# Optimization experiments

Measured on AMD Instinct MI355X. Metric: run time of the kernel, lower is better.

Reference implementation:

```python
import jax, jax.numpy as jnp
import numpy as np


def _scan_dir(x, A, B, reverse):
    """First-order linear recurrence h_i = A*h_{i-1} + B*x_i along last axis (W).
    x: [Bsz, C, H, W]; A, B: [C]. reverse=True scans right-to-left but returns
    states in original index order (matching torch scan_backward)."""
    xs = jnp.moveaxis(x, -1, 0)  # [W, Bsz, C, H]
    Ab = A[None, :, None]
    Bb = B[None, :, None]
    def step(h, xi):
        h = Ab * h + Bb * xi
        return h, h
    h0 = jnp.zeros_like(xs[0])
    _, hs = jax.lax.scan(step, h0, xs, reverse=reverse)
    return jnp.moveaxis(hs, 0, -1)  # [Bsz, C, H, W]


def _conv1x1(x, W, b):
    # x: [B,Cin,H,W], W: [Cout,Cin], b: [Cout]
    return jnp.einsum('bchw,dc->bdhw', x, W) + b[None, :, None, None]


def setup_inputs() -> dict:
    key = jax.random.key(0)
    ks = jax.random.split(key, 10)
    B, C, H, W = 8, 64, 128, 128
    D = 128  # hidden_dim
    return {
        'F_in': jax.random.normal(ks[0], (B, C, H, W), dtype=jnp.float32),
        'prior': jax.random.uniform(ks[1], (B, 1, H, W), dtype=jnp.float32),
        'Wi': jax.random.normal(ks[2], (D, C), dtype=jnp.float32) * 0.05,
        'bi': jnp.zeros((D,), dtype=jnp.float32),
        'A_param': jax.random.normal(ks[3], (D,), dtype=jnp.float32),
        'B_param': jax.random.normal(ks[4], (D,), dtype=jnp.float32),
        'alpha': jnp.float32(0.1),
        'gamma': jnp.float32(0.1),
        'Wf': jax.random.normal(ks[5], (D, 4 * D), dtype=jnp.float32) * 0.05,
        'bf': jnp.zeros((D,), dtype=jnp.float32),
        'Wo': jax.random.normal(ks[6], (C, D), dtype=jnp.float32) * 0.05,
        'bo': jnp.zeros((C,), dtype=jnp.float32),
    }


def reference(F_in, prior, Wi, bi, A_param, B_param, alpha, gamma, Wf, bf, Wo, bo):
    # prior has 1 channel, repeated to C channels (prior already matches HxW)
    prior_r = jnp.broadcast_to(prior, F_in.shape)
    F_mod = F_in + alpha * prior_r
    x = _conv1x1(F_mod, Wi, bi)  # [B, D, H, W]
    A = jnp.tanh(A_param)
    Bp = B_param
    h_lr = _scan_dir(x, A, Bp, reverse=False)
    h_rl = _scan_dir(x, A, Bp, reverse=True)
    xt = jnp.swapaxes(x, 2, 3)  # scan over H axis
    h_tb = jnp.swapaxes(_scan_dir(xt, A, Bp, reverse=False), 2, 3)
    h_bt = jnp.swapaxes(_scan_dir(xt, A, Bp, reverse=True), 2, 3)
    h = jnp.concatenate([h_lr, h_rl, h_tb, h_bt], axis=1)  # [B, 4D, H, W]
    h = _conv1x1(h, Wf, bf)   # fusion -> [B, D, H, W]
    out = _conv1x1(h, Wo, bo)  # output_proj -> [B, C, H, W]
    return F_mod + gamma * out
```

## Files before the change

### kernel.cpp

```cpp
#include <hip/hip_runtime.h>
#include <hip/hip_bf16.h>

typedef unsigned int u32;
typedef unsigned short u16;
typedef float f32x2 __attribute__((ext_vector_type(2)));
typedef float f32x4 __attribute__((ext_vector_type(4)));
using bf16x8 = __attribute__((ext_vector_type(8))) short;
using f32x4v = __attribute__((ext_vector_type(4))) float;

#define DEVINL __device__ __forceinline__

constexpr int SCAN_LDS = 32768;
constexpr int XS = 132;
constexpr int LDS_X = 128 * XS * 2;

DEVINL float bf2f(u16 u) { union { u32 i; float f; } v; v.i = ((u32)u) << 16; return v.f; }
DEVINL float bf2f_lo(u32 u) { union { u32 i; float f; } v; v.i = u << 16; return v.f; }
DEVINL float bf2f_hi(u32 u) { union { u32 i; float f; } v; v.i = u & 0xffff0000u; return v.f; }
DEVINL u16 f2bf(float f) {
  __hip_bfloat16 h = __float2bfloat16(f);
  u16 r; __builtin_memcpy(&r, &h, 2); return r;
}
DEVINL u32 pack2(float a, float b) { return (u32)f2bf(a) | ((u32)f2bf(b) << 16); }

__global__ __launch_bounds__(256) void k_pre(
    const float* __restrict__ Wf, const float* __restrict__ Wo,
    const float* __restrict__ bf_, const float* __restrict__ bo,
    const float* __restrict__ A_param, const float* __restrict__ Wi,
    float* __restrict__ A_t, float* __restrict__ beff,
    u16* __restrict__ Mrow, u16* __restrict__ Wi_bf) {
  const int wg = blockIdx.x, t = threadIdx.x;
  if (wg < 128) {
    const int idx = wg * 256 + t;
    const int cout = idx >> 9;
    const int k = idx & 511;
    float s = 0.f;
    for (int d = 0; d < 128; ++d) s = fmaf(Wo[cout * 128 + d], Wf[d * 512 + k], s);
    const int dir = k >> 7, dm = k & 127;
    Mrow[(dir * 64 + cout) * 128 + dm] = f2bf(s);
  } else if (wg == 128) {
    if (t < 128) A_t[t] = tanhf(A_param[t]);
    if (t < 64) {
      float s = bo[t];
      for (int d = 0; d < 128; ++d) s = fmaf(Wo[t * 128 + d], bf_[d], s);
      beff[t] = s;
    }
  } else {
#pragma unroll
    for (int k = 0; k < 32; ++k) {
      const int i = t + k * 256;
      Wi_bf[i] = f2bf(Wi[i]);
    }
  }
}

extern __shared__ char smem[];

template <bool REV>
DEVINL void scan_local(char* buf, int dp, int chunk, f32x2 A2, f32x2 B2) {
  f32x2 h = { 0.f, 0.f };
  const u32 cb = (u32)(dp * 4);
  const int s = chunk * 32;
  u32 nx[8];
#pragma unroll
  for (int j = 0; j < 8; ++j) {
    const int i = REV ? (127 - (s + j)) : (s + j);
    nx[j] = *(const u32*)(buf + i * 128 + (cb ^ ((u32)((i & 7) << 4))));
  }
  for (int ib = 0; ib < 32; ib += 8) {
    u32 cur[8];
#pragma unroll
    for (int j = 0; j < 8; ++j) cur[j] = nx[j];
    if (ib + 8 < 32) {
#pragma unroll
      for (int j = 0; j < 8; ++j) {
        const int i2 = s + ib + 8 + j;
        const int i = REV ? (127 - i2) : i2;
        nx[j] = *(const u32*)(buf + i * 128 + (cb ^ ((u32)((i & 7) << 4))));
      }
    }
#pragma unroll
    for (int j = 0; j < 8; ++j) {
      const int i2 = s + ib + j;
      const int i = REV ? (127 - i2) : i2;
      const f32x2 xv = { bf2f_lo(cur[j]), bf2f_hi(cur[j]) };
      h = A2 * h + B2 * xv;
      *(u32*)(buf + i * 128 + (cb ^ ((u32)((i & 7) << 4)))) = pack2(h.x, h.y);
    }
  }
}

template <bool REV>
DEVINL void scan_fix(char* buf, int dp, int chunk, f32x2 A2) {
  if (chunk == 0) return;
  f32x2 q = A2;
#pragma unroll
  for (int k = 0; k < 5; ++k) q *= q;
  const u32 cb = (u32)(dp * 4);
  f32x2 C = { 0.f, 0.f };
  for (int k = 0; k < chunk; ++k) {
    const int i2 = k * 32 + 31;
    const int i = REV ? (127 - i2) : i2;
    const u32 v = *(const u32*)(buf + i * 128 + (cb ^ ((u32)((i & 7) << 4))));
    const f32x2 xv = { bf2f_lo(v), bf2f_hi(v) };
    C = C * q + xv;
  }
  f32x2 p = A2;
  const int s = chunk * 32;
  u32 nx[8];
#pragma unroll
  for (int j = 0; j < 8; ++j) {
    const int i = REV ? (127 - (s + j)) : (s + j);
    nx[j] = *(const u32*)(buf + i * 128 + (cb ^ ((u32)((i & 7) << 4))));
  }
  for (int ib = 0; ib < 32; ib += 8) {
    u32 cur[8];
#pragma unroll
    for (int j = 0; j < 8; ++j) cur[j] = nx[j];
    if (ib + 8 < 32) {
#pragma unroll
      for (int j = 0; j < 8; ++j) {
        const int i2 = s + ib + 8 + j;
        const int i = REV ? (127 - i2) : i2;
        nx[j] = *(const u32*)(buf + i * 128 + (cb ^ ((u32)((i & 7) << 4))));
      }
    }
#pragma unroll
    for (int j = 0; j < 8; ++j) {
      const int i2 = s + ib + j;
      const int i = REV ? (127 - i2) : i2;
      const f32x2 xv = { bf2f_lo(cur[j]), bf2f_hi(cur[j]) };
      const f32x2 hv = p * C + xv;
      *(u32*)(buf + i * 128 + (cb ^ ((u32)((i & 7) << 4)))) = pack2(hv.x, hv.y);
      p *= A2;
    }
  }
}

DEVINL void run_scans(char* bufA, char* bufB, int t, int e,
                      const float* __restrict__ A_t, const float* __restrict__ Bp) {
  const int dp = t & 31, chunk = (t >> 5) & 3, dir = t >> 7;
  const int dgp = e * 64 + dp * 2;
  const f32x2 a = *(const f32x2*)(A_t + dgp);
  const f32x2 bb = *(const f32x2*)(Bp + dgp);
  char* sb = dir ? bufB : bufA;
  if (dir == 0) scan_local<false>(sb, dp, chunk, a, bb);
  else          scan_local<true >(sb, dp, chunk, a, bb);
  __syncthreads();
  if (dir == 0) scan_fix<false>(sb, dp, chunk, a);
  else          scan_fix<true >(sb, dp, chunk, a);
}

DEVINL void combine64(const char* buf, const u16* __restrict__ Mrow, int dir, int e,
                      int lane, int wv, f32x4v (&acc2)[4][2]) {
  const int l15 = lane & 15, kg = lane >> 4;
#pragma unroll
  for (int ks = 0; ks < 2; ++ks) {
    bf16x8 afr[4], bfr[2];
#pragma unroll
    for (int ct = 0; ct < 4; ++ct)
      afr[ct] = *(const bf16x8*)(Mrow + ((size_t)dir * 64 + ct * 16 + l15) * 128 + e * 64 + ks * 32 + kg * 8);
#pragma unroll
    for (int pt = 0; pt < 2; ++pt) {
      const int row = wv * 32 + pt * 16 + l15;
      bfr[pt] = *(const bf16x8*)(buf + row * 128 + ((u32)(ks * 64 + kg * 16) ^ ((u32)((row & 7) << 4))));
    }
#pragma unroll
    for (int ct = 0; ct < 4; ++ct)
#pragma unroll
      for (int pt = 0; pt < 2; ++pt)
        acc2[ct][pt] = __builtin_amdgcn_mfma_f32_16x16x32_bf16(bfr[pt], afr[ct], acc2[ct][pt], 0, 0, 0);
  }
}

DEVINL void acc_to_outs(const f32x4v (&acc2)[4][2], int lane, int wv, char* buf) {
  const int l15 = lane & 15, kg = lane >> 4;
#pragma unroll
  for (int ct = 0; ct < 4; ++ct)
#pragma unroll
    for (int pt = 0; pt < 2; ++pt) {
      const int c = ct * 16 + l15;
      const int pos = wv * 32 + pt * 16 + kg * 4;
      *(f32x4v*)(buf + c * 512 + ((u32)(pos * 4) ^ ((u32)((c & 7) << 4)))) = acc2[ct][pt];
    }
}

DEVINL void outs_to_global(const char* buf, u16* __restrict__ og, int t) {
#pragma unroll
  for (int j = 0; j < 16; ++j) {
    const int i = t + j * 256;
    const int c = i >> 6, p2 = (i & 63) * 2;
    const f32x2 v = *(const f32x2*)(buf + c * 512 + ((u32)(p2 * 4) ^ ((u32)((c & 7) << 4))));
    *(u32*)(og + c * 128 + p2) = pack2(v.x, v.y);
  }
}

__global__ __launch_bounds__(256, 5) void k_A(
    const float* __restrict__ F_in, const float* __restrict__ prior,
    const u16* __restrict__ Wi_bf, const float* __restrict__ bi,
    const float* __restrict__ Bp, const float* __restrict__ alpha_p,
    const float* __restrict__ A_t, const u16* __restrict__ Mrow,
    u16* __restrict__ x2, u16* __restrict__ Shp) {
  char* bufA = smem;
  char* bufB = smem + 16384;

  const int t = threadIdx.x;
  const int lane = t & 63, wv = t >> 6, l15 = lane & 15, kg = lane >> 4;
  const int bid = blockIdx.x;
  const int b = bid >> 8, h = (bid >> 1) & 127, e = bid & 1;

  {
    const int w = t & 127, ch = t >> 7;
    const float alpha = alpha_p[0];
    const float pv = prior[(b * 128 + h) * 128 + w];
    const float* Fb = F_in + ((size_t)b * 64 + ch * 32) * 16384 + h * 128 + w;
    const u32 sw = (u32)((w & 7) << 4);
    char* rowp = bufA + w * 128;
#pragma unroll
    for (int q = 0; q < 4; ++q) {
      float fv[8];
#pragma unroll
      for (int j = 0; j < 8; ++j) fv[j] = fmaf(alpha, pv, Fb[(q * 8 + j) * 16384]);
      uint4 pk;
      pk.x = pack2(fv[0], fv[1]); pk.y = pack2(fv[2], fv[3]);
      pk.z = pack2(fv[4], fv[5]); pk.w = pack2(fv[6], fv[7]);
      *(uint4*)(rowp + ((u32)(ch * 64 + q * 16) ^ sw)) = pk;
    }
  }
  __syncthreads();

  bf16x8 bF[2][2];
#pragma unroll
  for (int wj = 0; wj < 2; ++wj)
#pragma unroll
    for (int ks = 0; ks < 2; ++ks) {
      const int row = wv * 32 + wj * 16 + l15;
      bF[wj][ks] = *(const bf16x8*)(bufA + row * 128 + ((u32)(ks * 64 + kg * 16) ^ ((u32)((row & 7) << 4))));
    }
  __syncthreads();

  {
    f32x4v acc[4][2];
#pragma unroll
    for (int dt = 0; dt < 4; ++dt) {
      const f32x4 bv = *(const f32x4*)(bi + e * 64 + dt * 16 + kg * 4);
      const f32x4v bvv = { bv.x, bv.y, bv.z, bv.w };
#pragma unroll
      for (int wj = 0; wj < 2; ++wj) acc[dt][wj] = bvv;
    }
#pragma unroll
    for (int ks = 0; ks < 2; ++ks)
#pragma unroll
      for (int dt = 0; dt < 4; ++dt) {
        const bf16x8 aWi = *(const bf16x8*)(Wi_bf + (e * 64 + dt * 16 + l15) * 64 + ks * 32 + kg * 8);
        acc[dt][0] = __builtin_amdgcn_mfma_f32_16x16x32_bf16(aWi, bF[0][ks], acc[dt][0], 0, 0, 0);
        acc[dt][1] = __builtin_amdgcn_mfma_f32_16x16x32_bf16(aWi, bF[1][ks], acc[dt][1], 0, 0, 0);
      }
#pragma unroll
    for (int dt = 0; dt < 4; ++dt)
#pragma unroll
      for (int wj = 0; wj < 2; ++wj) {
        const int w = wv * 32 + wj * 16 + l15;
        const int dl = dt * 16 + kg * 4;
        uint2 pk;
        pk.x = pack2(acc[dt][wj][0], acc[dt][wj][1]);
        pk.y = pack2(acc[dt][wj][2], acc[dt][wj][3]);
        *(uint2*)(bufA + w * 128 + ((u32)(dl * 2) ^ ((u32)((w & 7) << 4)))) = pk;
      }
  }
  __syncthreads();

  {
    u16* xg = x2 + (size_t)bid * 8192;
#pragma unroll
    for (int j = 0; j < 4; ++j) {
      const int idx = t + j * 256;
      const int row = idx >> 3, q = idx & 7;
      const u32 off = (u32)(q * 16) ^ ((u32)((row & 7) << 4));
      const uint4 v = *(const uint4*)(bufA + row * 128 + off);
      *(uint4*)(xg + row * 64 + q * 8) = v;
      *(uint4*)(bufB + row * 128 + off) = v;
    }
  }
  __syncthreads();

  run_scans(bufA, bufB, t, e, A_t, Bp);
  __syncthreads();

  f32x4v acc2[4][2];
#pragma unroll
  for (int i = 0; i < 4; ++i)
#pragma unroll
    for (int j = 0; j < 2; ++j) acc2[i][j] = (f32x4v)0.f;
  combine64(bufA, Mrow, 0, e, lane, wv, acc2);
  combine64(bufB, Mrow, 1, e, lane, wv, acc2);
  __syncthreads();

  acc_to_outs(acc2, lane, wv, smem);
  __syncthreads();

  outs_to_global(smem, Shp + (size_t)bid * 8192, t);
}

__global__ __launch_bounds__(256, 5) void k_B(
    const u16* __restrict__ x2, const float* __restrict__ Bp,
    const float* __restrict__ A_t, const u16* __restrict__ Mrow,
    u16* __restrict__ Svp) {
  char* bufA = smem;
  char* bufB = smem + 16384;
  const int t = threadIdx.x;
  const int lane = t & 63, wv = t >> 6;
  const int bid = blockIdx.x;
  const int b = bid >> 8, w = (bid >> 1) & 127, e = bid & 1;

#pragma unroll
  for (int j = 0; j < 4; ++j) {
    const int idx = t + j * 256;
    const int hh = idx >> 3, q = idx & 7;
    const uint4 v = *(const uint4*)(x2 + ((size_t)((b * 128 + hh) * 2 + e)) * 8192 + w * 64 + q * 8);
    const u32 col = (u32)(q * 16) ^ ((u32)((hh & 7) << 4));
    *(uint4*)(bufA + hh * 128 + col) = v;
    *(uint4*)(bufB + hh * 128 + col) = v;
  }
  __syncthreads();

  run_scans(bufA, bufB, t, e, A_t, Bp);
  __syncthreads();

  f32x4v acc2[4][2];
#pragma unroll
  for (int i = 0; i < 4; ++i)
#pragma unroll
    for (int j = 0; j < 2; ++j) acc2[i][j] = (f32x4v)0.f;
  combine64(bufA, Mrow, 2, e, lane, wv, acc2);
  combine64(bufB, Mrow, 3, e, lane, wv, acc2);
  __syncthreads();

  acc_to_outs(acc2, lane, wv, smem);
  __syncthreads();

  outs_to_global(smem, Svp + (size_t)bid * 8192, t);
}

__global__ __launch_bounds__(256) void k_final(
    const float* __restrict__ F_in, const float* __restrict__ prior,
    const float* __restrict__ alpha_p, const float* __restrict__ gamma_p,
    const float* __restrict__ beff, const u16* __restrict__ Svp,
    const u16* __restrict__ Shp, float* __restrict__ out) {
  u16* Xu = (u16*)smem;
  const int t = threadIdx.x;
  const int bid = blockIdx.x, b = bid >> 6, c = bid & 63;
  const size_t base = (size_t)bid * 16384;

  for (int i = t; i < 2048; i += 256) {
    const int w = i >> 4, q = i & 15;
    const u16* s0 = Svp + ((size_t)((b * 128 + w) * 2)) * 8192 + c * 128 + q * 8;
    const uint4 a4 = *(const uint4*)(s0);
    const uint4 b4 = *(const uint4*)(s0 + 8192);
    const u16* ap = (const u16*)&a4;
    const u16* bp = (const u16*)&b4;
    u32* dst = (u32*)(Xu + w * 132 + q * 8);
#pragma unroll
    for (int k = 0; k < 4; ++k) {
      const float lo = bf2f(ap[k * 2]) + bf2f(bp[k * 2]);
      const float hi = bf2f(ap[k * 2 + 1]) + bf2f(bp[k * 2 + 1]);
      dst[k] = pack2(lo, hi);
    }
  }
  __syncthreads();
  const float alpha = alpha_p[0], gamma = gamma_p[0];
  const float be = beff[c];
  for (int i = t; i < 2048; i += 256) {
    const int hh = i >> 4, w8 = (i & 15) * 8;
    const size_t off = base + hh * 128 + w8;
    const u16* sh0 = Shp + ((size_t)((b * 128 + hh) * 2)) * 8192 + c * 128 + w8;
    const uint4 g0 = *(const uint4*)(sh0);
    const uint4 g1 = *(const uint4*)(sh0 + 8192);
    const u16* p0 = (const u16*)&g0;
    const u16* p1 = (const u16*)&g1;
    const float* Fp = F_in + off;
    float* Op = out + off;
    const float* Pp = prior + (b * 128 + hh) * 128 + w8;
#pragma unroll
    for (int q = 0; q < 8; ++q) {
      const float sv = bf2f(Xu[(w8 + q) * 132 + hh]);
      Op[q] = Fp[q] + alpha * Pp[q] + gamma * (bf2f(p0[q]) + bf2f(p1[q]) + sv + be);
    }
  }
}

extern "C" void kernel_launch(void* const* d_in, const int* in_sizes, int n_in,
                              void* d_out, int out_size, void* d_ws, size_t ws_size,
                              hipStream_t stream) {
  const float* F_in   = (const float*)d_in[0];
  const float* prior  = (const float*)d_in[1];
  const float* Wi     = (const float*)d_in[2];
  const float* bi     = (const float*)d_in[3];
  const float* A_par  = (const float*)d_in[4];
  const float* B_par  = (const float*)d_in[5];
  const float* alpha  = (const float*)d_in[6];
  const float* gamma  = (const float*)d_in[7];
  const float* Wf     = (const float*)d_in[8];
  const float* bf_    = (const float*)d_in[9];
  const float* Wo     = (const float*)d_in[10];
  const float* bo     = (const float*)d_in[11];
  float* out = (float*)d_out;

  char* ws = (char*)d_ws;
  float* A_t   = (float*)ws;
  float* beff  = (float*)(ws + 512);
  u16*   Mrow  = (u16*)(ws + 1024);
  u16*   Wi_bf = (u16*)(ws + 66560);
  u16*   x2    = (u16*)(ws + 82944);
  u16*   Shp   = (u16*)(ws + 82944 + 33554432);
  u16*   Svp   = (u16*)(ws + 82944 + 67108864);

  hipFuncSetAttribute((const void*)k_A, hipFuncAttributeMaxDynamicSharedMemorySize, SCAN_LDS);
  hipFuncSetAttribute((const void*)k_B, hipFuncAttributeMaxDynamicSharedMemorySize, SCAN_LDS);

  k_pre  <<<130, 256, 0, stream>>>(Wf, Wo, bf_, bo, A_par, Wi, A_t, beff, Mrow, Wi_bf);
  k_A    <<<2048, 256, SCAN_LDS, stream>>>(F_in, prior, Wi_bf, bi, B_par, alpha, A_t, Mrow, x2, Shp);
  k_B    <<<2048, 256, SCAN_LDS, stream>>>(x2, B_par, A_t, Mrow, Svp);
  k_final<<<512, 256, LDS_X, stream>>>(F_in, prior, alpha, gamma, beff, Svp, Shp, out);
}
```

Baseline: 98.13 us.

## Split input projection into own kernel and merge horizontal/vertical scans into one launch

The input projection (prior add, bf16 convert, MFMA against Wi) moves into a separate kernel k_x. It computes all 128 hidden channels per row and writes x2 in a [b,h,w,128] layout. The horizontal and vertical scans then run together in one 4096-block kernel, with odd/even blocks choosing the scan direction. This gives better load balance and overlap between the two scan kinds, and the F_in staging no longer sits inside the scan kernel. In exchange, the horizontal scans now re-read x from global memory and the F_in load is no longer shared with the scan work.

```diff
diff --git a/kernel.cpp b/kernel.cpp
--- a/kernel.cpp
+++ b/kernel.cpp
@@ -10,6 +10,7 @@
 
 #define DEVINL __device__ __forceinline__
 
+constexpr int XLDS = 16384;
 constexpr int SCAN_LDS = 32768;
 constexpr int XS = 132;
 constexpr int LDS_X = 128 * XS * 2;
@@ -56,6 +57,77 @@
 
 extern __shared__ char smem[];
 
+__global__ __launch_bounds__(256, 4) void k_x(
+    const float* __restrict__ F_in, const float* __restrict__ prior,
+    const u16* __restrict__ Wi_bf, const float* __restrict__ bi,
+    const float* __restrict__ alpha_p, u16* __restrict__ x2) {
+  char* FT = smem;
+
+  const int t = threadIdx.x;
+  const int lane = t & 63, wv = t >> 6, l15 = lane & 15, kg = lane >> 4;
+  const int bid = blockIdx.x, b = bid >> 7, h = bid & 127;
+
+  {
+    const int w = t & 127, ch = t >> 7;
+    const float alpha = alpha_p[0];
+    const float pv = prior[(b * 128 + h) * 128 + w];
+    const float* Fb = F_in + ((size_t)b * 64 + ch * 32) * 16384 + h * 128 + w;
+    const u32 sw = (u32)((w & 7) << 4);
+    char* rowp = FT + w * 128;
+#pragma unroll
+    for (int q = 0; q < 4; ++q) {
+      float fv[8];
+#pragma unroll
+      for (int j = 0; j < 8; ++j) fv[j] = fmaf(alpha, pv, Fb[(q * 8 + j) * 16384]);
+      uint4 pk;
+      pk.x = pack2(fv[0], fv[1]); pk.y = pack2(fv[2], fv[3]);
+      pk.z = pack2(fv[4], fv[5]); pk.w = pack2(fv[6], fv[7]);
+      *(uint4*)(rowp + ((u32)(ch * 64 + q * 16) ^ sw)) = pk;
+    }
+  }
+  __syncthreads();
+
+  bf16x8 bF[2][2];
+#pragma unroll
+  for (int wj = 0; wj < 2; ++wj)
+#pragma unroll
+    for (int ks = 0; ks < 2; ++ks) {
+      const int row = wv * 32 + wj * 16 + l15;
+      bF[wj][ks] = *(const bf16x8*)(FT + row * 128 + ((u32)(ks * 64 + kg * 16) ^ ((u32)((row & 7) << 4))));
+    }
+
+  {
+    f32x4v acc[8][2];
+#pragma unroll
+    for (int dt = 0; dt < 8; ++dt) {
+      const f32x4 bv = *(const f32x4*)(bi + dt * 16 + kg * 4);
+      const f32x4v bvv = { bv.x, bv.y, bv.z, bv.w };
+#pragma unroll
+      for (int wj = 0; wj < 2; ++wj) acc[dt][wj] = bvv;
+    }
+#pragma unroll
+    for (int ks = 0; ks < 2; ++ks)
+#pragma unroll
+      for (int dt = 0; dt < 8; ++dt) {
+        const bf16x8 aWi = *(const bf16x8*)(Wi_bf + (dt * 16 + l15) * 64 + ks * 32 + kg * 8);
+        acc[dt][0] = __builtin_amdgcn_mfma_f32_16x16x32_bf16(aWi, bF[0][ks], acc[dt][0], 0, 0, 0);
+        acc[dt][1] = __builtin_amdgcn_mfma_f32_16x16x32_bf16(aWi, bF[1][ks], acc[dt][1], 0, 0, 0);
+      }
+    u16* xg = x2 + (size_t)(b * 128 + h) * 16384;
+#pragma unroll
+    for (int dt = 0; dt < 8; ++dt)
+#pragma unroll
+      for (int wj = 0; wj < 2; ++wj) {
+        const int w = wv * 32 + wj * 16 + l15;
+        const int dl = dt * 16 + kg * 4;
+        uint2 pk;
+        pk.x = pack2(acc[dt][wj][0], acc[dt][wj][1]);
+        pk.y = pack2(acc[dt][wj][2], acc[dt][wj][3]);
+        *(uint2*)(xg + w * 128 + dl) = pk;
+      }
+  }
+}
+
 template <bool REV>
 DEVINL void scan_local(char* buf, int dp, int chunk, f32x2 A2, f32x2 B2) {
   f32x2 h = { 0.f, 0.f };
@@ -195,132 +267,30 @@
   }
 }
 
-__global__ __launch_bounds__(256, 5) void k_A(
-    const float* __restrict__ F_in, const float* __restrict__ prior,
-    const u16* __restrict__ Wi_bf, const float* __restrict__ bi,
-    const float* __restrict__ Bp, const float* __restrict__ alpha_p,
-    const float* __restrict__ A_t, const u16* __restrict__ Mrow,
-    u16* __restrict__ x2, u16* __restrict__ Shp) {
-  char* bufA = smem;
-  char* bufB = smem + 16384;
-
-  const int t = threadIdx.x;
-  const int lane = t & 63, wv = t >> 6, l15 = lane & 15, kg = lane >> 4;
-  const int bid = blockIdx.x;
-  const int b = bid >> 8, h = (bid >> 1) & 127, e = bid & 1;
-
-  {
-    const int w = t & 127, ch = t >> 7;
-    const float alpha = alpha_p[0];
-    const float pv = prior[(b * 128 + h) * 128 + w];
-    const float* Fb = F_in + ((size_t)b * 64 + ch * 32) * 16384 + h * 128 + w;
-    const u32 sw = (u32)((w & 7) << 4);
-    char* rowp = bufA + w * 128;
-#pragma unroll
-    for (int q = 0; q < 4; ++q) {
-      float fv[8];
-#pragma unroll
-      for (int j = 0; j < 8; ++j) fv[j] = fmaf(alpha, pv, Fb[(q * 8 + j) * 16384]);
-      uint4 pk;
-      pk.x = pack2(fv[0], fv[1]); pk.y = pack2(fv[2], fv[3]);
-      pk.z = pack2(fv[4], fv[5]); pk.w = pack2(fv[6], fv[7]);
-      *(uint4*)(rowp + ((u32)(ch * 64 + q * 16) ^ sw)) = pk;
-    }
-  }
-  __syncthreads();
-
-  bf16x8 bF[2][2];
-#pragma unroll
-  for (int wj = 0; wj < 2; ++wj)
-#pragma unroll
-    for (int ks = 0; ks < 2; ++ks) {
-      const int row = wv * 32 + wj * 16 + l15;
-      bF[wj][ks] = *(const bf16x8*)(bufA + row * 128 + ((u32)(ks * 64 + kg * 16) ^ ((u32)((row & 7) << 4))));
-    }
-  __syncthreads();
-
-  {
-    f32x4v acc[4][2];
-#pragma unroll
-    for (int dt = 0; dt < 4; ++dt) {
-      const f32x4 bv = *(const f32x4*)(bi + e * 64 + dt * 16 + kg * 4);
-      const f32x4v bvv = { bv.x, bv.y, bv.z, bv.w };
-#pragma unroll
-      for (int wj = 0; wj < 2; ++wj) acc[dt][wj] = bvv;
-    }
-#pragma unroll
-    for (int ks = 0; ks < 2; ++ks)
-#pragma unroll
-      for (int dt = 0; dt < 4; ++dt) {
-        const bf16x8 aWi = *(const bf16x8*)(Wi_bf + (e * 64 + dt * 16 + l15) * 64 + ks * 32 + kg * 8);
-        acc[dt][0] = __builtin_amdgcn_mfma_f32_16x16x32_bf16(aWi, bF[0][ks], acc[dt][0], 0, 0, 0);
-        acc[dt][1] = __builtin_amdgcn_mfma_f32_16x16x32_bf16(aWi, bF[1][ks], acc[dt][1], 0, 0, 0);
-      }
-#pragma unroll
-    for (int dt = 0; dt < 4; ++dt)
-#pragma unroll
-      for (int wj = 0; wj < 2; ++wj) {
-        const int w = wv * 32 + wj * 16 + l15;
-        const int dl = dt * 16 + kg * 4;
-        uint2 pk;
-        pk.x = pack2(acc[dt][wj][0], acc[dt][wj][1]);
-        pk.y = pack2(acc[dt][wj][2], acc[dt][wj][3]);
-        *(uint2*)(bufA + w * 128 + ((u32)(dl * 2) ^ ((u32)((w & 7) << 4)))) = pk;
-      }
-  }
-  __syncthreads();
-
-  {
-    u16* xg = x2 + (size_t)bid * 8192;
-#pragma unroll
-    for (int j = 0; j < 4; ++j) {
-      const int idx = t + j * 256;
-      const int row = idx >> 3, q = idx & 7;
-      const u32 off = (u32)(q * 16) ^ ((u32)((row & 7) << 4));
-      const uint4 v = *(const uint4*)(bufA + row * 128 + off);
-      *(uint4*)(xg + row * 64 + q * 8) = v;
-      *(uint4*)(bufB + row * 128 + off) = v;
-    }
-  }
-  __syncthreads();
-
-  run_scans(bufA, bufB, t, e, A_t, Bp);
-  __syncthreads();
-
-  f32x4v acc2[4][2];
-#pragma unroll
-  for (int i = 0; i < 4; ++i)
-#pragma unroll
-    for (int j = 0; j < 2; ++j) acc2[i][j] = (f32x4v)0.f;
-  combine64(bufA, Mrow, 0, e, lane, wv, acc2);
-  combine64(bufB, Mrow, 1, e, lane, wv, acc2);
-  __syncthreads();
-
-  acc_to_outs(acc2, lane, wv, smem);
-  __syncthreads();
-
-  outs_to_global(smem, Shp + (size_t)bid * 8192, t);
-}
-
-__global__ __launch_bounds__(256, 5) void k_B(
+__global__ __launch_bounds__(256, 5) void k_scan(
     const u16* __restrict__ x2, const float* __restrict__ Bp,
     const float* __restrict__ A_t, const u16* __restrict__ Mrow,
-    u16* __restrict__ Svp) {
+    u16* __restrict__ Shp, u16* __restrict__ Svp) {
   char* bufA = smem;
   char* bufB = smem + 16384;
   const int t = threadIdx.x;
   const int lane = t & 63, wv = t >> 6;
   const int bid = blockIdx.x;
-  const int b = bid >> 8, w = (bid >> 1) & 127, e = bid & 1;
+  const int vert = bid & 1;
+  const int bid2 = bid >> 1;
+  const int b = bid2 >> 8, p = (bid2 >> 1) & 127, e = bid2 & 1;
 
 #pragma unroll
   for (int j = 0; j < 4; ++j) {
     const int idx = t + j * 256;
-    const int hh = idx >> 3, q = idx & 7;
-    const uint4 v = *(const uint4*)(x2 + ((size_t)((b * 128 + hh) * 2 + e)) * 8192 + w * 64 + q * 8);
-    const u32 col = (u32)(q * 16) ^ ((u32)((hh & 7) << 4));
-    *(uint4*)(bufA + hh * 128 + col) = v;
-    *(uint4*)(bufB + hh * 128 + col) = v;
+    const int row = idx >> 3, q = idx & 7;
+    const u16* src = vert
+        ? x2 + (size_t)(b * 128 + row) * 16384 + p * 128 + e * 64 + q * 8
+        : x2 + (size_t)(b * 128 + p) * 16384 + row * 128 + e * 64 + q * 8;
+    const uint4 v = *(const uint4*)src;
+    const u32 col = (u32)(q * 16) ^ ((u32)((row & 7) << 4));
+    *(uint4*)(bufA + row * 128 + col) = v;
+    *(uint4*)(bufB + row * 128 + col) = v;
   }
   __syncthreads();
 
@@ -332,14 +302,15 @@
   for (int i = 0; i < 4; ++i)
 #pragma unroll
     for (int j = 0; j < 2; ++j) acc2[i][j] = (f32x4v)0.f;
-  combine64(bufA, Mrow, 2, e, lane, wv, acc2);
-  combine64(bufB, Mrow, 3, e, lane, wv, acc2);
+  combine64(bufA, Mrow, vert ? 2 : 0, e, lane, wv, acc2);
+  combine64(bufB, Mrow, vert ? 3 : 1, e, lane, wv, acc2);
   __syncthreads();
 
   acc_to_outs(acc2, lane, wv, smem);
   __syncthreads();
 
-  outs_to_global(smem, Svp + (size_t)bid * 8192, t);
+  u16* og = (vert ? Svp : Shp) + (size_t)bid2 * 8192;
+  outs_to_global(smem, og, t);
 }
 
 __global__ __launch_bounds__(256) void k_final(
@@ -415,11 +386,11 @@
   u16*   Shp   = (u16*)(ws + 82944 + 33554432);
   u16*   Svp   = (u16*)(ws + 82944 + 67108864);
 
-  hipFuncSetAttribute((const void*)k_A, hipFuncAttributeMaxDynamicSharedMemorySize, SCAN_LDS);
-  hipFuncSetAttribute((const void*)k_B, hipFuncAttributeMaxDynamicSharedMemorySize, SCAN_LDS);
+  hipFuncSetAttribute((const void*)k_x,    hipFuncAttributeMaxDynamicSharedMemorySize, XLDS);
+  hipFuncSetAttribute((const void*)k_scan, hipFuncAttributeMaxDynamicSharedMemorySize, SCAN_LDS);
 
   k_pre  <<<130, 256, 0, stream>>>(Wf, Wo, bf_, bo, A_par, Wi, A_t, beff, Mrow, Wi_bf);
-  k_A    <<<2048, 256, SCAN_LDS, stream>>>(F_in, prior, Wi_bf, bi, B_par, alpha, A_t, Mrow, x2, Shp);
-  k_B    <<<2048, 256, SCAN_LDS, stream>>>(x2, B_par, A_t, Mrow, Svp);
+  k_x    <<<1024, 256, XLDS, stream>>>(F_in, prior, Wi_bf, bi, alpha, x2);
+  k_scan <<<4096, 256, SCAN_LDS, stream>>>(x2, B_par, A_t, Mrow, Shp, Svp);
   k_final<<<512, 256, LDS_X, stream>>>(F_in, prior, alpha, gamma, beff, Svp, Shp, out);
 }
```

Result: slower. 103.8 us (+5.8%).

## Fold B into conv output and rework scans as 16-element chunks over four channels

Applied to the files above, without the earlier changes.

The B coefficient is now multiplied into the input projection in k_A, so the stored x2 holds B*x. This lets both scan phases drop the B multiply, and k_B loses its Bp argument. The scan is reorganized so each thread handles four channels over 16-element chunks (8 chunks instead of 4). It loads all 16 values up front with 64-bit LDS reads, computes, then writes them back, which shortens the serial dependency chain and the fix-up chain. The duplicate copy into bufB now happens in the MFMA epilogue rather than in a separate pass. The trade-off is more registers per thread and a longer carry loop in the fix phase.

```diff
diff --git a/kernel.cpp b/kernel.cpp
--- a/kernel.cpp
+++ b/kernel.cpp
@@ -57,98 +57,84 @@
 extern __shared__ char smem[];
 
 template <bool REV>
-DEVINL void scan_local(char* buf, int dp, int chunk, f32x2 A2, f32x2 B2) {
-  f32x2 h = { 0.f, 0.f };
-  const u32 cb = (u32)(dp * 4);
-  const int s = chunk * 32;
-  u32 nx[8];
-#pragma unroll
-  for (int j = 0; j < 8; ++j) {
-    const int i = REV ? (127 - (s + j)) : (s + j);
-    nx[j] = *(const u32*)(buf + i * 128 + (cb ^ ((u32)((i & 7) << 4))));
-  }
-  for (int ib = 0; ib < 32; ib += 8) {
-    u32 cur[8];
-#pragma unroll
-    for (int j = 0; j < 8; ++j) cur[j] = nx[j];
-    if (ib + 8 < 32) {
-#pragma unroll
-      for (int j = 0; j < 8; ++j) {
-        const int i2 = s + ib + 8 + j;
-        const int i = REV ? (127 - i2) : i2;
-        nx[j] = *(const u32*)(buf + i * 128 + (cb ^ ((u32)((i & 7) << 4))));
-      }
-    }
-#pragma unroll
-    for (int j = 0; j < 8; ++j) {
-      const int i2 = s + ib + j;
-      const int i = REV ? (127 - i2) : i2;
-      const f32x2 xv = { bf2f_lo(cur[j]), bf2f_hi(cur[j]) };
-      h = A2 * h + B2 * xv;
-      *(u32*)(buf + i * 128 + (cb ^ ((u32)((i & 7) << 4)))) = pack2(h.x, h.y);
-    }
+DEVINL void scan16(char* buf, int dq, int chunk, f32x2 a01, f32x2 a23) {
+  const u32 cb = (u32)(dq * 8);
+  const int s = chunk * 16;
+  uint2 v[16];
+#pragma unroll
+  for (int j = 0; j < 16; ++j) {
+    const int i2 = s + j;
+    const int i = REV ? (127 - i2) : i2;
+    v[j] = *(const uint2*)(buf + i * 128 + (cb ^ ((u32)((i & 7) << 4))));
+  }
+  f32x2 h01 = { 0.f, 0.f }, h23 = { 0.f, 0.f };
+#pragma unroll
+  for (int j = 0; j < 16; ++j) {
+    const f32x2 x0 = { bf2f_lo(v[j].x), bf2f_hi(v[j].x) };
+    const f32x2 x1 = { bf2f_lo(v[j].y), bf2f_hi(v[j].y) };
+    h01 = a01 * h01 + x0;
+    h23 = a23 * h23 + x1;
+    v[j].x = pack2(h01.x, h01.y);
+    v[j].y = pack2(h23.x, h23.y);
+  }
+#pragma unroll
+  for (int j = 0; j < 16; ++j) {
+    const int i2 = s + j;
+    const int i = REV ? (127 - i2) : i2;
+    *(uint2*)(buf + i * 128 + (cb ^ ((u32)((i & 7) << 4)))) = v[j];
   }
 }
 
 template <bool REV>
-DEVINL void scan_fix(char* buf, int dp, int chunk, f32x2 A2) {
+DEVINL void fix16(char* buf, int dq, int chunk, f32x2 a01, f32x2 a23) {
   if (chunk == 0) return;
-  f32x2 q = A2;
-#pragma unroll
-  for (int k = 0; k < 5; ++k) q *= q;
-  const u32 cb = (u32)(dp * 4);
-  f32x2 C = { 0.f, 0.f };
+  f32x2 q01 = a01, q23 = a23;
+#pragma unroll
+  for (int k = 0; k < 4; ++k) { q01 *= q01; q23 *= q23; }
+  const u32 cb = (u32)(dq * 8);
+  f32x2 C01 = { 0.f, 0.f }, C23 = { 0.f, 0.f };
   for (int k = 0; k < chunk; ++k) {
-    const int i2 = k * 32 + 31;
+    const int i2 = k * 16 + 15;
     const int i = REV ? (127 - i2) : i2;
-    const u32 v = *(const u32*)(buf + i * 128 + (cb ^ ((u32)((i & 7) << 4))));
-    const f32x2 xv = { bf2f_lo(v), bf2f_hi(v) };
-    C = C * q + xv;
-  }
-  f32x2 p = A2;
-  const int s = chunk * 32;
-  u32 nx[8];
-#pragma unroll
-  for (int j = 0; j < 8; ++j) {
-    const int i = REV ? (127 - (s + j)) : (s + j);
-    nx[j] = *(const u32*)(buf + i * 128 + (cb ^ ((u32)((i & 7) << 4))));
-  }
-  for (int ib = 0; ib < 32; ib += 8) {
-    u32 cur[8];
-#pragma unroll
-    for (int j = 0; j < 8; ++j) cur[j] = nx[j];
-    if (ib + 8 < 32) {
-#pragma unroll
-      for (int j = 0; j < 8; ++j) {
-        const int i2 = s + ib + 8 + j;
-        const int i = REV ? (127 - i2) : i2;
-        nx[j] = *(const u32*)(buf + i * 128 + (cb ^ ((u32)((i & 7) << 4))));
-      }
-    }
-#pragma unroll
-    for (int j = 0; j < 8; ++j) {
-      const int i2 = s + ib + j;
-      const int i = REV ? (127 - i2) : i2;
-      const f32x2 xv = { bf2f_lo(cur[j]), bf2f_hi(cur[j]) };
-      const f32x2 hv = p * C + xv;
-      *(u32*)(buf + i * 128 + (cb ^ ((u32)((i & 7) << 4)))) = pack2(hv.x, hv.y);
-      p *= A2;
-    }
-  }
-}
-
-DEVINL void run_scans(char* bufA, char* bufB, int t, int e,
-                      const float* __restrict__ A_t, const float* __restrict__ Bp) {
-  const int dp = t & 31, chunk = (t >> 5) & 3, dir = t >> 7;
-  const int dgp = e * 64 + dp * 2;
-  const f32x2 a = *(const f32x2*)(A_t + dgp);
-  const f32x2 bb = *(const f32x2*)(Bp + dgp);
+    const uint2 v = *(const uint2*)(buf + i * 128 + (cb ^ ((u32)((i & 7) << 4))));
+    C01 = C01 * q01 + (f32x2){ bf2f_lo(v.x), bf2f_hi(v.x) };
+    C23 = C23 * q23 + (f32x2){ bf2f_lo(v.y), bf2f_hi(v.y) };
+  }
+  const int s = chunk * 16;
+  uint2 v[16];
+#pragma unroll
+  for (int j = 0; j < 16; ++j) {
+    const int i2 = s + j;
+    const int i = REV ? (127 - i2) : i2;
+    v[j] = *(const uint2*)(buf + i * 128 + (cb ^ ((u32)((i & 7) << 4))));
+  }
+  f32x2 p01 = a01, p23 = a23;
+#pragma unroll
+  for (int j = 0; j < 16; ++j) {
+    const f32x2 h0 = p01 * C01 + (f32x2){ bf2f_lo(v[j].x), bf2f_hi(v[j].x) };
+    const f32x2 h1 = p23 * C23 + (f32x2){ bf2f_lo(v[j].y), bf2f_hi(v[j].y) };
+    v[j].x = pack2(h0.x, h0.y);
+    v[j].y = pack2(h1.x, h1.y);
+    p01 *= a01; p23 *= a23;
+  }
+#pragma unroll
+  for (int j = 0; j < 16; ++j) {
+    const int i2 = s + j;
+    const int i = REV ? (127 - i2) : i2;
+    *(uint2*)(buf + i * 128 + (cb ^ ((u32)((i & 7) << 4)))) = v[j];
+  }
+}
+
+DEVINL void run_scans(char* bufA, char* bufB, int t, int e, const float* __restrict__ A_t) {
+  const int dq = t & 15, chunk = (t >> 4) & 7, dir = t >> 7;
+  const f32x2 a01 = *(const f32x2*)(A_t + e * 64 + dq * 4);
+  const f32x2 a23 = *(const f32x2*)(A_t + e * 64 + dq * 4 + 2);
   char* sb = dir ? bufB : bufA;
-  if (dir == 0) scan_local<false>(sb, dp, chunk, a, bb);
-  else          scan_local<true >(sb, dp, chunk, a, bb);
-  __syncthreads();
-  if (dir == 0) scan_fix<false>(sb, dp, chunk, a);
-  else          scan_fix<true >(sb, dp, chunk, a);
+  if (dir == 0) scan16<false>(sb, dq, chunk, a01, a23);
+  else          scan16<true >(sb, dq, chunk, a01, a23);
+  __syncthreads();
+  if (dir == 0) fix16<false>(sb, dq, chunk, a01, a23);
+  else          fix16<true >(sb, dq, chunk, a01, a23);
 }
 
 DEVINL void combine64(const char* buf, const u16* __restrict__ Mrow, int dir, int e,
@@ -257,16 +243,22 @@
         acc[dt][1] = __builtin_amdgcn_mfma_f32_16x16x32_bf16(aWi, bF[1][ks], acc[dt][1], 0, 0, 0);
       }
 #pragma unroll
-    for (int dt = 0; dt < 4; ++dt)
+    for (int dt = 0; dt < 4; ++dt) {
+      const f32x4 B4 = *(const f32x4*)(Bp + e * 64 + dt * 16 + kg * 4);
+      const f32x4v B4v = { B4.x, B4.y, B4.z, B4.w };
 #pragma unroll
       for (int wj = 0; wj < 2; ++wj) {
+        const f32x4v sv = acc[dt][wj] * B4v;
         const int w = wv * 32 + wj * 16 + l15;
         const int dl = dt * 16 + kg * 4;
         uint2 pk;
-        pk.x = pack2(acc[dt][wj][0], acc[dt][wj][1]);
-        pk.y = pack2(acc[dt][wj][2], acc[dt][wj][3]);
-        *(uint2*)(bufA + w * 128 + ((u32)(dl * 2) ^ ((u32)((w & 7) << 4)))) = pk;
+        pk.x = pack2(sv[0], sv[1]);
+        pk.y = pack2(sv[2], sv[3]);
+        const u32 col = (u32)(dl * 2) ^ ((u32)((w & 7) << 4));
+        *(uint2*)(bufA + w * 128 + col) = pk;
+        *(uint2*)(bufB + w * 128 + col) = pk;
       }
+    }
   }
   __syncthreads();
 
@@ -276,15 +268,13 @@
     for (int j = 0; j < 4; ++j) {
       const int idx = t + j * 256;
       const int row = idx >> 3, q = idx & 7;
-      const u32 off = (u32)(q * 16) ^ ((u32)((row & 7) << 4));
-      const uint4 v = *(const uint4*)(bufA + row * 128 + off);
+      const uint4 v = *(const uint4*)(bufA + row * 128 + ((u32)(q * 16) ^ ((u32)((row & 7) << 4))));
       *(uint4*)(xg + row * 64 + q * 8) = v;
-      *(uint4*)(bufB + row * 128 + off) = v;
-    }
-  }
-  __syncthreads();
-
-  run_scans(bufA, bufB, t, e, A_t, Bp);
+    }
+  }
+  __syncthreads();
+
+  run_scans(bufA, bufB, t, e, A_t);
   __syncthreads();
 
   f32x4v acc2[4][2];
@@ -303,7 +293,7 @@
 }
 
 __global__ __launch_bounds__(256, 5) void k_B(
-    const u16* __restrict__ x2, const float* __restrict__ Bp,
+    const u16* __restrict__ x2,
     const float* __restrict__ A_t, const u16* __restrict__ Mrow,
     u16* __restrict__ Svp) {
   char* bufA = smem;
@@ -324,7 +314,7 @@
   }
   __syncthreads();
 
-  run_scans(bufA, bufB, t, e, A_t, Bp);
+  run_scans(bufA, bufB, t, e, A_t);
   __syncthreads();
 
   f32x4v acc2[4][2];
@@ -420,6 +410,6 @@
 
   k_pre  <<<130, 256, 0, stream>>>(Wf, Wo, bf_, bo, A_par, Wi, A_t, beff, Mrow, Wi_bf);
   k_A    <<<2048, 256, SCAN_LDS, stream>>>(F_in, prior, Wi_bf, bi, B_par, alpha, A_t, Mrow, x2, Shp);
-  k_B    <<<2048, 256, SCAN_LDS, stream>>>(x2, B_par, A_t, Mrow, Svp);
+  k_B    <<<2048, 256, SCAN_LDS, stream>>>(x2, A_t, Mrow, Svp);
   k_final<<<512, 256, LDS_X, stream>>>(F_in, prior, alpha, gamma, beff, Svp, Shp, out);
 }
```

New measurement: 100.8 us. 1.03x slower.
